# Kernel optimization log

Hardware: AMD Instinct MI355X
Metric: run time of the kernel (lower is better)

Reference implementation:

```python
import jax, jax.numpy as jnp
import numpy as np

B, C, NX, NY = 8, 128, 256, 256
N = 32768

def setup_inputs() -> dict:
    key = jax.random.key(0)
    k1, k2 = jax.random.split(key)
    x = jax.random.normal(k1, (B, C, NX, NY), dtype=jnp.float32)
    coords = jax.random.uniform(k2, (B, N, 2), dtype=jnp.float32)
    return {"x": x, "coords": coords}

def reference(x, coords):
    b, c, nx, ny = x.shape
    # Match torch: scale by (dim-1), clamp to [0, dim], floor to int (nearest-lower gather).
    px = jnp.clip(coords[:, :, 1] * (nx - 1), 0, nx).astype(jnp.int32)  # (b, n)
    py = jnp.clip(coords[:, :, 0] * (ny - 1), 0, ny).astype(jnp.int32)  # (b, n)
    # Direct per-batch gather: out[b, c, n] = x[b, c, px[b,n], py[b,n]]
    flat_idx = px * ny + py                                             # (b, n)
    x_flat = x.reshape(b, c, nx * ny)                                   # (b, c, nx*ny)
    out = jnp.take_along_axis(x_flat, flat_idx[:, None, :], axis=2)     # (b, c, n)
    return out
```

## Files before the change

### kernel.cpp

```cpp
#include <hip/hip_runtime.h>
#include <hip/hip_bf16.h>

#define B_  8
#define C_  128
#define NX_ 256
#define NY_ 256
#define N_  32768
#define PLANE_ (NX_ * NY_)
#define CG_  8
#define NCG_ (C_ / CG_)
#define NBLK_ (N_ / 256)

__global__ __launch_bounds__(256) void nu_grid_sampler_kernel(
    const float* __restrict__ x,
    const float* __restrict__ coords,
    float* __restrict__ out)
{
    const int bid  = blockIdx.x;
    const int b    = bid & 7;
    const int rem  = bid >> 3;
    const int cg   = rem >> 7;
    const int nblk = rem & (NBLK_ - 1);

    const int n  = nblk * 256 + threadIdx.x;
    const int c0 = cg * CG_;

    const float2 cc = *reinterpret_cast<const float2*>(coords + ((size_t)b * N_ + n) * 2);
    const float cy = cc.x;
    const float cx = cc.y;

    const int px = (int)fminf(fmaxf(cx * (float)(NX_ - 1), 0.0f), (float)NX_);
    const int py = (int)fminf(fmaxf(cy * (float)(NY_ - 1), 0.0f), (float)NY_);
    const int idx = min(px * NY_ + py, PLANE_ - 1);

    const float* __restrict__ xb = x + ((size_t)b * C_ + c0) * PLANE_ + idx;
    float* __restrict__ ob = out + ((size_t)b * C_ + c0) * N_ + n;

    float v0 = xb[(size_t)0 * PLANE_];
    float v1 = xb[(size_t)1 * PLANE_];
    float v2 = xb[(size_t)2 * PLANE_];
    float v3 = xb[(size_t)3 * PLANE_];
    float v4 = xb[(size_t)4 * PLANE_];
    float v5 = xb[(size_t)5 * PLANE_];
    float v6 = xb[(size_t)6 * PLANE_];
    float v7 = xb[(size_t)7 * PLANE_];
    __builtin_nontemporal_store(v0, ob + (size_t)0 * N_);
    __builtin_nontemporal_store(v1, ob + (size_t)1 * N_);
    __builtin_nontemporal_store(v2, ob + (size_t)2 * N_);
    __builtin_nontemporal_store(v3, ob + (size_t)3 * N_);
    __builtin_nontemporal_store(v4, ob + (size_t)4 * N_);
    __builtin_nontemporal_store(v5, ob + (size_t)5 * N_);
    __builtin_nontemporal_store(v6, ob + (size_t)6 * N_);
    __builtin_nontemporal_store(v7, ob + (size_t)7 * N_);
}

extern "C" void kernel_launch(void* const* d_in, const int* in_sizes, int n_in,
                              void* d_out, int out_size, void* d_ws, size_t ws_size,
                              hipStream_t stream) {
    const float* x      = (const float*)d_in[0];
    const float* coords = (const float*)d_in[1];
    float* out          = (float*)d_out;

    dim3 block(256);
    dim3 grid(B_ * NCG_ * NBLK_);
    nu_grid_sampler_kernel<<<grid, block, 0, stream>>>(x, coords, out);
}
```

Before: 489.9 us.

## Gather via bitmap-marked channel-last transpose of sampled pixels

Adds a three-pass path: mark sampled pixels in a bitmap, transpose x to a pixel-major layout writing only marked pixels, then gather contiguous channel vectors per sample through shared memory and write coalesced output. The aim is to replace strided per-channel scattered reads with contiguous reads. The cost is reading all of x once (256MB) plus extra launches, a memset and a large workspace. If the workspace is too small it falls back to the original kernel.

```diff
diff --git a/kernel.cpp b/kernel.cpp
--- a/kernel.cpp
+++ b/kernel.cpp
@@ -7,51 +7,102 @@
 #define NY_ 256
 #define N_  32768
 #define PLANE_ (NX_ * NY_)
-#define CG_  8
-#define NCG_ (C_ / CG_)
-#define NBLK_ (N_ / 256)
+#define XT_BYTES ((size_t)B_ * PLANE_ * C_ * 4)
+#define BM_WORDS_PER_B (PLANE_ / 32)
+#define BM_BYTES ((size_t)B_ * BM_WORDS_PER_B * 4)
 
-__global__ __launch_bounds__(256) void nu_grid_sampler_kernel(
-    const float* __restrict__ x,
-    const float* __restrict__ coords,
-    float* __restrict__ out)
-{
+__device__ __forceinline__ int sample_idx(const float* __restrict__ coords, int b, int n) {
+    const float2 cc = *reinterpret_cast<const float2*>(coords + ((size_t)b * N_ + n) * 2);
+    const int px = (int)fminf(fmaxf(cc.y * (float)(NX_ - 1), 0.0f), (float)NX_);
+    const int py = (int)fminf(fmaxf(cc.x * (float)(NY_ - 1), 0.0f), (float)NY_);
+    return min(px * NY_ + py, PLANE_ - 1);
+}
+
+__global__ __launch_bounds__(256) void mark_kernel(const float* __restrict__ coords,
+                                                   unsigned* __restrict__ bm) {
+    const int n = blockIdx.x * 256 + threadIdx.x;
+    const int b = blockIdx.y;
+    const int idx = sample_idx(coords, b, n);
+    atomicOr(&bm[b * BM_WORDS_PER_B + (idx >> 5)], 1u << (idx & 31));
+}
+
+__global__ __launch_bounds__(256) void transpose_kernel(const float* __restrict__ x,
+                                                        const unsigned* __restrict__ bm,
+                                                        float* __restrict__ xT) {
+    __shared__ float tile[32][129];
+    const int bid = blockIdx.x;
+    const int b   = bid & 7;
+    const int p0  = (bid >> 3) << 5;
+    const int t   = threadIdx.x;
+
+    const float* __restrict__ xb = x + (size_t)b * C_ * PLANE_;
+    const int pl = t & 31, cr = t >> 5;
+    #pragma unroll
+    for (int r = 0; r < 16; ++r) {
+        const int c = r * 8 + cr;
+        tile[pl][c] = xb[(size_t)c * PLANE_ + p0 + pl];
+    }
+    __syncthreads();
+
+    float* __restrict__ xTb = xT + (size_t)b * PLANE_ * C_;
+    const int c = t & 127, ph = t >> 7;
+    #pragma unroll
+    for (int r = 0; r < 16; ++r) {
+        const int p = r * 2 + ph;
+        const unsigned w = bm[b * BM_WORDS_PER_B + ((p0 + p) >> 5)];
+        if (w & (1u << ((p0 + p) & 31)))
+            xTb[(size_t)(p0 + p) * C_ + c] = tile[p][c];
+    }
+}
+
+__global__ __launch_bounds__(256) void gather_kernel(const float* __restrict__ xT,
+                                                     const float* __restrict__ coords,
+                                                     float* __restrict__ out) {
+    __shared__ float smp[64][130];
+    __shared__ int   sidx[64];
+    const int bid = blockIdx.x;
+    const int b   = bid & 7;
+    const int n0  = (bid >> 3) << 6;
+    const int t   = threadIdx.x;
+
+    if (t < 64) sidx[t] = sample_idx(coords, b, n0 + t);
+    __syncthreads();
+
+    const float* __restrict__ xTb = xT + (size_t)b * PLANE_ * C_;
+    const int g = t & 63, sr = t >> 6;
+    #pragma unroll
+    for (int r = 0; r < 16; ++r) {
+        const int s = r * 4 + sr;
+        const float2 v = *reinterpret_cast<const float2*>(&xTb[(size_t)sidx[s] * C_ + 2 * g]);
+        *reinterpret_cast<float2*>(&smp[s][2 * g]) = v;
+    }
+    __syncthreads();
+
+    float* __restrict__ ob = out + (size_t)b * C_ * N_ + n0;
+    const int s = t & 63, ch = t >> 6;
+    #pragma unroll
+    for (int r = 0; r < 32; ++r) {
+        const int c = r * 4 + ch;
+        __builtin_nontemporal_store(smp[s][c], ob + (size_t)c * N_ + s);
+    }
+}
+
+__global__ __launch_bounds__(256) void fallback_kernel(const float* __restrict__ x,
+                                                       const float* __restrict__ coords,
+                                                       float* __restrict__ out) {
     const int bid  = blockIdx.x;
     const int b    = bid & 7;
     const int rem  = bid >> 3;
     const int cg   = rem >> 7;
-    const int nblk = rem & (NBLK_ - 1);
-
+    const int nblk = rem & 127;
     const int n  = nblk * 256 + threadIdx.x;
-    const int c0 = cg * CG_;
-
-    const float2 cc = *reinterpret_cast<const float2*>(coords + ((size_t)b * N_ + n) * 2);
-    const float cy = cc.x;
-    const float cx = cc.y;
-
-    const int px = (int)fminf(fmaxf(cx * (float)(NX_ - 1), 0.0f), (float)NX_);
-    const int py = (int)fminf(fmaxf(cy * (float)(NY_ - 1), 0.0f), (float)NY_);
-    const int idx = min(px * NY_ + py, PLANE_ - 1);
-
+    const int c0 = cg * 8;
+    const int idx = sample_idx(coords, b, n);
     const float* __restrict__ xb = x + ((size_t)b * C_ + c0) * PLANE_ + idx;
     float* __restrict__ ob = out + ((size_t)b * C_ + c0) * N_ + n;
-
-    float v0 = xb[(size_t)0 * PLANE_];
-    float v1 = xb[(size_t)1 * PLANE_];
-    float v2 = xb[(size_t)2 * PLANE_];
-    float v3 = xb[(size_t)3 * PLANE_];
-    float v4 = xb[(size_t)4 * PLANE_];
-    float v5 = xb[(size_t)5 * PLANE_];
-    float v6 = xb[(size_t)6 * PLANE_];
-    float v7 = xb[(size_t)7 * PLANE_];
-    __builtin_nontemporal_store(v0, ob + (size_t)0 * N_);
-    __builtin_nontemporal_store(v1, ob + (size_t)1 * N_);
-    __builtin_nontemporal_store(v2, ob + (size_t)2 * N_);
-    __builtin_nontemporal_store(v3, ob + (size_t)3 * N_);
-    __builtin_nontemporal_store(v4, ob + (size_t)4 * N_);
-    __builtin_nontemporal_store(v5, ob + (size_t)5 * N_);
-    __builtin_nontemporal_store(v6, ob + (size_t)6 * N_);
-    __builtin_nontemporal_store(v7, ob + (size_t)7 * N_);
+    #pragma unroll
+    for (int i = 0; i < 8; ++i)
+        __builtin_nontemporal_store(xb[(size_t)i * PLANE_], ob + (size_t)i * N_);
 }
 
 extern "C" void kernel_launch(void* const* d_in, const int* in_sizes, int n_in,
@@ -61,7 +112,14 @@
     const float* coords = (const float*)d_in[1];
     float* out          = (float*)d_out;
 
-    dim3 block(256);
-    dim3 grid(B_ * NCG_ * NBLK_);
-    nu_grid_sampler_kernel<<<grid, block, 0, stream>>>(x, coords, out);
+    if (ws_size >= XT_BYTES + BM_BYTES) {
+        float*    xT = (float*)d_ws;
+        unsigned* bm = (unsigned*)((char*)d_ws + XT_BYTES);
+        hipMemsetAsync(bm, 0, BM_BYTES, stream);
+        mark_kernel<<<dim3(N_ / 256, B_), 256, 0, stream>>>(coords, bm);
+        transpose_kernel<<<B_ * (PLANE_ / 32), 256, 0, stream>>>(x, bm, xT);
+        gather_kernel<<<B_ * (N_ / 64), 256, 0, stream>>>(xT, coords, out);
+    } else {
+        fallback_kernel<<<B_ * 16 * 128, 256, 0, stream>>>(x, coords, out);
+    }
 }
```

New measurement: 460.6 us. -6.0%, faster.
